# Kernel optimization log

Measured on AMD Instinct MI355X. Metric: run time of the kernel, lower is better.

Reference implementation:

```python
import jax, jax.numpy as jnp
import numpy as np
from jax import lax

N, CIN, P, CH, COUT = 1024, 3, 14, 256, 3
DN = ('NCHW', 'OIHW', 'NCHW')


def _conv(x, w, b, pad=1):
    y = lax.conv_general_dilated(x, w, (1, 1), [(pad, pad), (pad, pad)], dimension_numbers=DN)
    return y + b[None, :, None, None]


def _conv_transpose(x, w_t, b):
    # PyTorch ConvTranspose2d(k=3, stride=2, padding=1, output_padding=1):
    # equivalent to conv with lhs_dilation=2, padding (k-1-p, k-1-p+op) = (1, 2),
    # kernel with in/out swapped and spatially flipped. w_t: [in, out, 3, 3]
    w = jnp.flip(jnp.transpose(w_t, (1, 0, 2, 3)), axis=(2, 3))  # [out, in, 3, 3]
    y = lax.conv_general_dilated(x, w, (1, 1), [(1, 2), (1, 2)], lhs_dilation=(2, 2),
                                 dimension_numbers=DN)
    return y + b[None, :, None, None]


def setup_inputs() -> dict:
    key = jax.random.key(0)
    ks = jax.random.split(key, 16)
    s3 = lambda cin: 1.0 / np.sqrt(cin * 9)
    inp = {"x": jax.random.normal(ks[0], (N, CIN, P, P), dtype=jnp.float32)}
    inp["w1"] = jax.random.normal(ks[1], (CH, CIN, 3, 3), jnp.float32) * s3(CIN)
    inp["b1"] = jnp.zeros((CH,), jnp.float32)
    inp["w2"] = jax.random.normal(ks[2], (CH, CH, 3, 3), jnp.float32) * s3(CH)
    inp["b2"] = jnp.zeros((CH,), jnp.float32)
    inp["w3"] = jax.random.normal(ks[3], (CH, CH, 3, 3), jnp.float32) * s3(CH)
    inp["b3"] = jnp.zeros((CH,), jnp.float32)
    inp["w4"] = jax.random.normal(ks[4], (CH, CH, 3, 3), jnp.float32) * s3(CH)
    inp["b4"] = jnp.zeros((CH,), jnp.float32)
    inp["wt"] = jax.random.normal(ks[5], (CH, CH, 3, 3), jnp.float32) * s3(CH)  # [in, out, kh, kw]
    inp["bt"] = jnp.zeros((CH,), jnp.float32)
    inp["w5"] = jax.random.normal(ks[6], (COUT, CH, 1, 1), jnp.float32) * (1.0 / np.sqrt(CH))
    inp["b5"] = jnp.zeros((COUT,), jnp.float32)
    return inp


def reference(x, w1, b1, w2, b2, w3, b3, w4, b4, wt, bt, w5, b5):
    h = jax.nn.relu(_conv(x, w1, b1))
    h = jax.nn.relu(_conv(h, w2, b2))
    h = jax.nn.relu(_conv(h, w3, b3))
    h = jax.nn.relu(_conv(h, w4, b4))
    h = jax.nn.relu(_conv_transpose(h, wt, bt))  # [N, 256, 2P, 2P]
    h = _conv(h, w5, b5, pad=0)                   # 1x1 conv -> [N, 3, 2P, 2P]
    return jax.nn.sigmoid(h)
```

## Files before the change

### kernel.cpp

```cpp
#include <hip/hip_runtime.h>
#include <hip/hip_fp16.h>

typedef _Float16 half8 __attribute__((ext_vector_type(8)));
typedef _Float16 half4 __attribute__((ext_vector_type(4)));
typedef float floatx4 __attribute__((ext_vector_type(4)));

#define PLANE 65536
#define PK_ELEMS 589824
#define GUARD 4096

__global__ void repack_kernel(const float* __restrict__ w2, const float* __restrict__ w3,
                              const float* __restrict__ w4, const float* __restrict__ wt,
                              _Float16* __restrict__ pk) {
    int t = blockIdx.x * 256 + threadIdx.x;
    int l = t & 63;
    int idx = t >> 6;
    int nt = idx & 15; idx >>= 4;
    int ks = idx & 7;  idx >>= 3;
    int tap = idx % 9;
    int layer = idx / 9;
    int co = nt * 16 + (l & 15);
    int ci0 = ks * 32 + (l >> 4) * 8;
    const float* w = (layer == 0) ? w2 : (layer == 1) ? w3 : (layer == 2) ? w4 : wt;
    _Float16* dst = pk + (size_t)layer * PK_ELEMS + (((size_t)(tap * 8 + ks) * 16 + nt) * 64 + l) * 8;
    if (layer < 3) {
        for (int j = 0; j < 8; ++j)
            dst[j] = (_Float16)w[(co * 256 + (ci0 + j)) * 9 + tap];
    } else {
        int ky = tap / 3, kx = tap % 3;
        for (int j = 0; j < 8; ++j)
            dst[j] = (_Float16)w[((ci0 + j) * 256 + co) * 9 + (2 - ky) * 3 + (2 - kx)];
    }
}

__global__ __launch_bounds__(1024, 4) void conv1_kernel(const float* __restrict__ x,
                                                        const float* __restrict__ w1,
                                                        const float* __restrict__ b1,
                                                        _Float16* __restrict__ act) {
    __shared__ float inl[3][16][16];
    __shared__ float lw[256 * 27];
    __shared__ float lb1[256];
    int n = blockIdx.x, tid = threadIdx.x;
    if (tid < 768) ((float*)inl)[tid] = 0.f;
    __syncthreads();
    for (int i = tid; i < 3 * 196; i += 1024) {
        int ci = i / 196, r = i % 196, y = r / 14, xx = r % 14;
        inl[ci][y + 1][xx + 1] = x[(size_t)n * 588 + i];
    }
    for (int i = tid; i < 256 * 27; i += 1024) lw[i] = w1[i];
    if (tid < 256) lb1[tid] = b1[tid];
    __syncthreads();
    int p = tid >> 2, q = tid & 3;
    int py = p >> 4, px = p & 15;
    _Float16* ga = act + (size_t)n * PLANE + p * 256;
    int sw = (p & 7) << 3;
    if (py == 0 || py == 15 || px == 0 || px == 15) {
        for (int ci = 0; ci < 64; ++ci) { int co = q + ci * 4; ga[co ^ sw] = (_Float16)0.f; }
    } else {
        float vin[27];
        #pragma unroll
        for (int ci = 0; ci < 3; ++ci)
            #pragma unroll
            for (int ky = 0; ky < 3; ++ky)
                #pragma unroll
                for (int kx = 0; kx < 3; ++kx)
                    vin[ci * 9 + ky * 3 + kx] = inl[ci][py - 1 + ky][px - 1 + kx];
        for (int ci = 0; ci < 64; ++ci) {
            int co = q + ci * 4;
            float acc = lb1[co];
            const float* wp = &lw[co * 27];
            #pragma unroll
            for (int k = 0; k < 27; ++k) acc += vin[k] * wp[k];
            ga[co ^ sw] = (_Float16)fmaxf(acc, 0.f);
        }
    }
}


#define INIT_ACC(BIASPTR)                                                        \
    {                                                                            \
        _Pragma("unroll")                                                        \
        for (int ni = 0; ni < 4; ++ni) {                                         \
            floatx4 bv;                                                          \
            _Pragma("unroll")                                                    \
            for (int reg = 0; reg < 4; ++reg)                                    \
                bv[reg] = (BIASPTR)[(cg * 4 + ni) * 16 + kg * 4 + reg];          \
            _Pragma("unroll")                                                    \
            for (int i = 0; i < 5; ++i) acc[i][ni] = bv;                         \
        }                                                                        \
    }

#define ACCUM_TAP(PKT, DOFF)                                                     \
    {                                                                            \
        const _Float16* pkt_ = (PKT);                                            \
        int poff_[5];                                                            \
        _Pragma("unroll")                                                        \
        for (int j = 0; j < 5; ++j) poff_[j] = (pp[j] + (DOFF)) * 256;           \
        half8 a_[4], an_[4], bb_[5];                                             \
        _Pragma("unroll")                                                        \
        for (int ni = 0; ni < 4; ++ni)                                           \
            a_[ni] = *(const half8*)(pkt_ + ((cg * 4 + ni) * 64 + lane) * 8);    \
        _Pragma("clang loop unroll(disable)")                                    \
        for (int ks = 0; ks < 8; ++ks) {                                         \
            int kk = (ks * 4 + kg) << 3;                                         \
            _Pragma("unroll")                                                    \
            for (int j = 0; j < 4; ++j)                                          \
                bb_[j] = *(const half8*)(plane + poff_[j] + (kk ^ ((poff_[j] >> 5) & 56))); \
            if (pg == 0 || pg == 1)                                              \
                bb_[4] = *(const half8*)(plane + poff_[4] + (kk ^ ((poff_[4] >> 5) & 56))); \
            if (ks < 7) {                                                        \
                _Pragma("unroll")                                                \
                for (int ni = 0; ni < 4; ++ni)                                   \
                    an_[ni] = *(const half8*)(pkt_ + (((ks + 1) * 16 + cg * 4 + ni) * 64 + lane) * 8); \
            }                                                                    \
            _Pragma("unroll")                                                    \
            for (int j = 0; j < 4; ++j) {                                        \
                acc[j][0] = __builtin_amdgcn_mfma_f32_16x16x32_f16(a_[0], bb_[j], acc[j][0], 0, 0, 0); \
                acc[j][1] = __builtin_amdgcn_mfma_f32_16x16x32_f16(a_[1], bb_[j], acc[j][1], 0, 0, 0); \
                acc[j][2] = __builtin_amdgcn_mfma_f32_16x16x32_f16(a_[2], bb_[j], acc[j][2], 0, 0, 0); \
                acc[j][3] = __builtin_amdgcn_mfma_f32_16x16x32_f16(a_[3], bb_[j], acc[j][3], 0, 0, 0); \
            }                                                                    \
            if (pg == 0 || pg == 1) {                                            \
                acc[4][0] = __builtin_amdgcn_mfma_f32_16x16x32_f16(a_[0], bb_[4], acc[4][0], 0, 0, 0); \
                acc[4][1] = __builtin_amdgcn_mfma_f32_16x16x32_f16(a_[1], bb_[4], acc[4][1], 0, 0, 0); \
                acc[4][2] = __builtin_amdgcn_mfma_f32_16x16x32_f16(a_[2], bb_[4], acc[4][2], 0, 0, 0); \
                acc[4][3] = __builtin_amdgcn_mfma_f32_16x16x32_f16(a_[3], bb_[4], acc[4][3], 0, 0, 0); \
            }                                                                    \
            if (ks < 7) {                                                        \
                _Pragma("unroll")                                                \
                for (int ni = 0; ni < 4; ++ni) a_[ni] = an_[ni];                 \
            }                                                                    \
        }                                                                        \
    }

#define EPILOGUE(RY, RX)                                                         \
    {                                                                            \
        _Pragma("unroll")                                                        \
        for (int i = 0; i < 5; ++i) {                                            \
            if (i < 4 || pg < 2) {                                               \
                float s0 = 0.f, s1 = 0.f, s2 = 0.f;                              \
                _Pragma("unroll")                                                \
                for (int ni = 0; ni < 4; ++ni) {                                 \
                    int co0 = (cg * 4 + ni) * 16 + kg * 4;                       \
                    _Pragma("unroll")                                            \
                    for (int reg = 0; reg < 4; ++reg) {                          \
                        float v = fmaxf(acc[i][ni][reg], 0.f);                   \
                        s0 += v * w5l[co0 + reg];                                \
                        s1 += v * w5l[256 + co0 + reg];                          \
                        s2 += v * w5l[512 + co0 + reg];                          \
                    }                                                            \
                }                                                                \
                s0 += __shfl_xor(s0, 16, 64); s0 += __shfl_xor(s0, 32, 64);      \
                s1 += __shfl_xor(s1, 16, 64); s1 += __shfl_xor(s1, 32, 64);      \
                s2 += __shfl_xor(s2, 16, 64); s2 += __shfl_xor(s2, 32, 64);      \
                if (lane < 16 && colok) {                                        \
                    int yy = pg + 3 * i;                              \
                    int pix = (2 * yy + (RY)) * 28 + 2 * (col - 1) + (RX);       \
                    atomicAdd(&o3[pix * 3 + 0], s0);                             \
                    atomicAdd(&o3[pix * 3 + 1], s1);                             \
                    atomicAdd(&o3[pix * 3 + 2], s2);                             \
                }                                                                \
            }                                                                    \
        }                                                                        \
    }

__global__ __launch_bounds__(768, 3) void fused_kernel(const _Float16* __restrict__ act,
                                                       const _Float16* __restrict__ pk,
                                                       const float* __restrict__ b2,
                                                       const float* __restrict__ b3,
                                                       const float* __restrict__ b4,
                                                       const float* __restrict__ bt,
                                                       const float* __restrict__ w5,
                                                       const float* __restrict__ b5,
                                                       float* __restrict__ out) {
    __shared__ _Float16 plane[PLANE + 2 * GUARD];
    __shared__ float o3[2352];
    __shared__ float w5l[768];
    int n = blockIdx.x, tid = threadIdx.x;
    const _Float16* ga = act + (size_t)n * PLANE;
    if (tid < 512) {
        int g = (tid < 256) ? tid : (tid - 256 + (PLANE + GUARD) / 8);
        *(uint4*)(plane + g * 8) = uint4{0, 0, 0, 0};
    }
    for (int i = tid; i < 8192; i += 768)
        *(uint4*)(plane + GUARD + i * 8) = *(const uint4*)(ga + i * 8);
    for (int i = tid; i < 2352; i += 768) o3[i] = b5[i % 3];
    w5l[tid] = w5[tid];

    int lane = tid & 63, wid = tid >> 6;
    int cg = wid & 3, pg = wid >> 2;
    int col = lane & 15, kg = lane >> 4;
    bool colok = (col >= 1 && col <= 14);

    int pp[5];
    #pragma unroll
    for (int i = 0; i < 5; ++i) pp[i] = (pg + 3 * i + 1) * 16 + col + 16;
    __syncthreads();

    floatx4 acc[5][4];

    for (int L = 0; L < 3; ++L) {
        const _Float16* pkL = pk + (size_t)L * PK_ELEMS;
        const float* bias = (L == 0) ? b2 : (L == 1) ? b3 : b4;
        INIT_ACC(bias)
        for (int tap = 0; tap < 9; ++tap) {
            int doff = (tap / 3) * 16 + (tap % 3) - 17;
            ACCUM_TAP(pkL + (size_t)tap * 65536, doff)
        }
        __syncthreads();
        #pragma unroll
        for (int i = 0; i < 5; ++i) {
            if (i < 4 || pg < 2) {
                int ppix = pp[i];
                int sw = (ppix & 7) << 3;
                if (colok) {
                    #pragma unroll
                    for (int ni = 0; ni < 4; ++ni) {
                        int co0 = (cg * 4 + ni) * 16 + kg * 4;
                        half4 h;
                        #pragma unroll
                        for (int reg = 0; reg < 4; ++reg) h[reg] = (_Float16)fmaxf(acc[i][ni][reg], 0.f);
                        *(half4*)(plane + ppix * 256 + (co0 ^ sw)) = h;
                    }
                }
            }
        }
        __syncthreads();
    }

    const _Float16* pkT = pk + (size_t)3 * PK_ELEMS;
    INIT_ACC(bt)
    ACCUM_TAP(pkT + 4 * 65536, 0)
    EPILOGUE(0, 0)
    INIT_ACC(bt)
    ACCUM_TAP(pkT + 3 * 65536, 0)
    ACCUM_TAP(pkT + 5 * 65536, 1)
    EPILOGUE(0, 1)
    INIT_ACC(bt)
    ACCUM_TAP(pkT + 1 * 65536, 0)
    ACCUM_TAP(pkT + 7 * 65536, 16)
    EPILOGUE(1, 0)
    INIT_ACC(bt)
    ACCUM_TAP(pkT + 0 * 65536, 0)
    ACCUM_TAP(pkT + 2 * 65536, 1)
    ACCUM_TAP(pkT + 6 * 65536, 16)
    ACCUM_TAP(pkT + 8 * 65536, 17)
    EPILOGUE(1, 1)

    __syncthreads();
    size_t ob = (size_t)n * 2352;
    for (int i = tid; i < 2352; i += 768) {
        int pix = i / 3, c = i % 3;
        float v = o3[i];
        out[ob + (size_t)c * 784 + pix] = 1.f / (1.f + __expf(-v));
    }
}

extern "C" void kernel_launch(void* const* d_in, const int* in_sizes, int n_in,
                              void* d_out, int out_size, void* d_ws, size_t ws_size,
                              hipStream_t stream) {
    const float* x  = (const float*)d_in[0];
    const float* w1 = (const float*)d_in[1];
    const float* b1 = (const float*)d_in[2];
    const float* w2 = (const float*)d_in[3];
    const float* b2 = (const float*)d_in[4];
    const float* w3 = (const float*)d_in[5];
    const float* b3 = (const float*)d_in[6];
    const float* w4 = (const float*)d_in[7];
    const float* b4 = (const float*)d_in[8];
    const float* wt = (const float*)d_in[9];
    const float* bt = (const float*)d_in[10];
    const float* w5 = (const float*)d_in[11];
    const float* b5 = (const float*)d_in[12];

    size_t need = ((size_t)1024 * PLANE + 4 * (size_t)PK_ELEMS) * sizeof(_Float16);
    if (ws_size < need) return;

    _Float16* act = (_Float16*)d_ws;
    _Float16* pk  = act + (size_t)1024 * PLANE;

    repack_kernel<<<1152, 256, 0, stream>>>(w2, w3, w4, wt, pk);
    conv1_kernel<<<1024, 1024, 0, stream>>>(x, w1, b1, act);
    fused_kernel<<<1024, 768, 0, stream>>>(act, pk, b2, b3, b4, bt, w5, b5, (float*)d_out);
}
```

Before: 1.026 ms.

## Switch fused conv MFMA tiles from 16x16x32 to 32x32x16 with repacked weights

Replaces the 16x16x32 f16 MFMA tiling with 32x32x16 instructions. Each wave now covers 64 output channels as two 32-wide tiles and two image rows per 32-pixel tile. The weight repack layout, accumulator shapes, bias init, LDS writeback and epilogue reduction are all reworked to match the new register layout, and weight loads are prefetched two k-steps ahead. The aim is fewer instructions and less LDS operand traffic per FLOP, at the cost of larger accumulator register pressure and extra wasted work on row edges.

New measurement: 1.292 ms. +26.0%, slower.

```diff
diff --git a/kernel.cpp b/kernel.cpp
--- a/kernel.cpp
+++ b/kernel.cpp
@@ -3,7 +3,7 @@
 
 typedef _Float16 half8 __attribute__((ext_vector_type(8)));
 typedef _Float16 half4 __attribute__((ext_vector_type(4)));
-typedef float floatx4 __attribute__((ext_vector_type(4)));
+typedef float floatx16 __attribute__((ext_vector_type(16)));
 
 #define PLANE 65536
 #define PK_ELEMS 589824
@@ -15,14 +15,14 @@
     int t = blockIdx.x * 256 + threadIdx.x;
     int l = t & 63;
     int idx = t >> 6;
-    int nt = idx & 15; idx >>= 4;
-    int ks = idx & 7;  idx >>= 3;
+    int ct = idx & 7;  idx >>= 3;
+    int ks = idx & 15; idx >>= 4;
     int tap = idx % 9;
     int layer = idx / 9;
-    int co = nt * 16 + (l & 15);
-    int ci0 = ks * 32 + (l >> 4) * 8;
+    int co  = ct * 32 + (l & 31);
+    int ci0 = ks * 16 + (l >> 5) * 8;
     const float* w = (layer == 0) ? w2 : (layer == 1) ? w3 : (layer == 2) ? w4 : wt;
-    _Float16* dst = pk + (size_t)layer * PK_ELEMS + (((size_t)(tap * 8 + ks) * 16 + nt) * 64 + l) * 8;
+    _Float16* dst = pk + (size_t)layer * PK_ELEMS + (((size_t)(tap * 16 + ks) * 8 + ct) * 64 + l) * 8;
     if (layer < 3) {
         for (int j = 0; j < 8; ++j)
             dst[j] = (_Float16)w[(co * 256 + (ci0 + j)) * 9 + tap];
@@ -80,55 +80,55 @@
 #define INIT_ACC(BIASPTR)                                                        \
     {                                                                            \
         _Pragma("unroll")                                                        \
-        for (int ni = 0; ni < 4; ++ni) {                                         \
-            floatx4 bv;                                                          \
+        for (int c = 0; c < 2; ++c) {                                            \
+            floatx16 bv;                                                         \
             _Pragma("unroll")                                                    \
-            for (int reg = 0; reg < 4; ++reg)                                    \
-                bv[reg] = (BIASPTR)[(cg * 4 + ni) * 16 + kg * 4 + reg];          \
-            _Pragma("unroll")                                                    \
-            for (int i = 0; i < 5; ++i) acc[i][ni] = bv;                         \
+            for (int reg = 0; reg < 16; ++reg)                                   \
+                bv[reg] = (BIASPTR)[(cg * 2 + c) * 32 + 4 * h + (reg & 3) + 8 * (reg >> 2)]; \
+            acc[0][c] = bv; acc[1][c] = bv; acc[2][c] = bv;                      \
         }                                                                        \
     }
 
 #define ACCUM_TAP(PKT, DOFF)                                                     \
     {                                                                            \
         const _Float16* pkt_ = (PKT);                                            \
-        int poff_[5];                                                            \
-        _Pragma("unroll")                                                        \
-        for (int j = 0; j < 5; ++j) poff_[j] = (pp[j] + (DOFF)) * 256;           \
-        half8 a_[4], an_[4], bb_[5];                                             \
-        _Pragma("unroll")                                                        \
-        for (int ni = 0; ni < 4; ++ni)                                           \
-            a_[ni] = *(const half8*)(pkt_ + ((cg * 4 + ni) * 64 + lane) * 8);    \
+        int poff_[3], swj_[3];                                                   \
+        _Pragma("unroll")                                                        \
+        for (int j = 0; j < 3; ++j) {                                            \
+            poff_[j] = (pp[j] + (DOFF)) * 256;                                   \
+            swj_[j] = (poff_[j] >> 5) & 56;                                      \
+        }                                                                        \
+        half8 a_[2], an_[2], a2_[2], bb_[3];                                     \
+        _Pragma("unroll")                                                        \
+        for (int c = 0; c < 2; ++c) {                                            \
+            a_[c]  = *(const half8*)(pkt_ + ((cg * 2 + c) * 64 + lane) * 8);     \
+            an_[c] = *(const half8*)(pkt_ + (((8) + cg * 2 + c) * 64 + lane) * 8); \
+        }                                                                        \
         _Pragma("clang loop unroll(disable)")                                    \
-        for (int ks = 0; ks < 8; ++ks) {                                         \
-            int kk = (ks * 4 + kg) << 3;                                         \
-            _Pragma("unroll")                                                    \
-            for (int j = 0; j < 4; ++j)                                          \
-                bb_[j] = *(const half8*)(plane + poff_[j] + (kk ^ ((poff_[j] >> 5) & 56))); \
-            if (pg == 0 || pg == 1)                                              \
-                bb_[4] = *(const half8*)(plane + poff_[4] + (kk ^ ((poff_[4] >> 5) & 56))); \
-            if (ks < 7) {                                                        \
+        for (int ks = 0; ks < 16; ++ks) {                                        \
+            int kk = ks * 16 + h8;                                               \
+            bb_[0] = *(const half8*)(plane + poff_[0] + (kk ^ swj_[0]));         \
+            bb_[1] = *(const half8*)(plane + poff_[1] + (kk ^ swj_[1]));         \
+            if (pg == 0)                                                         \
+                bb_[2] = *(const half8*)(plane + poff_[2] + (kk ^ swj_[2]));     \
+            if (ks < 14) {                                                       \
                 _Pragma("unroll")                                                \
-                for (int ni = 0; ni < 4; ++ni)                                   \
-                    an_[ni] = *(const half8*)(pkt_ + (((ks + 1) * 16 + cg * 4 + ni) * 64 + lane) * 8); \
-            }                                                                    \
-            _Pragma("unroll")                                                    \
-            for (int j = 0; j < 4; ++j) {                                        \
-                acc[j][0] = __builtin_amdgcn_mfma_f32_16x16x32_f16(a_[0], bb_[j], acc[j][0], 0, 0, 0); \
-                acc[j][1] = __builtin_amdgcn_mfma_f32_16x16x32_f16(a_[1], bb_[j], acc[j][1], 0, 0, 0); \
-                acc[j][2] = __builtin_amdgcn_mfma_f32_16x16x32_f16(a_[2], bb_[j], acc[j][2], 0, 0, 0); \
-                acc[j][3] = __builtin_amdgcn_mfma_f32_16x16x32_f16(a_[3], bb_[j], acc[j][3], 0, 0, 0); \
-            }                                                                    \
-            if (pg == 0 || pg == 1) {                                            \
-                acc[4][0] = __builtin_amdgcn_mfma_f32_16x16x32_f16(a_[0], bb_[4], acc[4][0], 0, 0, 0); \
-                acc[4][1] = __builtin_amdgcn_mfma_f32_16x16x32_f16(a_[1], bb_[4], acc[4][1], 0, 0, 0); \
-                acc[4][2] = __builtin_amdgcn_mfma_f32_16x16x32_f16(a_[2], bb_[4], acc[4][2], 0, 0, 0); \
-                acc[4][3] = __builtin_amdgcn_mfma_f32_16x16x32_f16(a_[3], bb_[4], acc[4][3], 0, 0, 0); \
-            }                                                                    \
-            if (ks < 7) {                                                        \
-                _Pragma("unroll")                                                \
-                for (int ni = 0; ni < 4; ++ni) a_[ni] = an_[ni];                 \
+                for (int c = 0; c < 2; ++c)                                      \
+                    a2_[c] = *(const half8*)(pkt_ + (((ks + 2) * 8 + cg * 2 + c) * 64 + lane) * 8); \
+            }                                                                    \
+            acc[0][0] = __builtin_amdgcn_mfma_f32_32x32x16_f16(a_[0], bb_[0], acc[0][0], 0, 0, 0); \
+            acc[0][1] = __builtin_amdgcn_mfma_f32_32x32x16_f16(a_[1], bb_[0], acc[0][1], 0, 0, 0); \
+            acc[1][0] = __builtin_amdgcn_mfma_f32_32x32x16_f16(a_[0], bb_[1], acc[1][0], 0, 0, 0); \
+            acc[1][1] = __builtin_amdgcn_mfma_f32_32x32x16_f16(a_[1], bb_[1], acc[1][1], 0, 0, 0); \
+            if (pg == 0) {                                                       \
+                acc[2][0] = __builtin_amdgcn_mfma_f32_32x32x16_f16(a_[0], bb_[2], acc[2][0], 0, 0, 0); \
+                acc[2][1] = __builtin_amdgcn_mfma_f32_32x32x16_f16(a_[1], bb_[2], acc[2][1], 0, 0, 0); \
+            }                                                                    \
+            if (ks < 14) {                                                       \
+                a_[0] = an_[0]; a_[1] = an_[1];                                  \
+                an_[0] = a2_[0]; an_[1] = a2_[1];                                \
+            } else {                                                             \
+                a_[0] = an_[0]; a_[1] = an_[1];                                  \
             }                                                                    \
         }                                                                        \
     }
@@ -136,25 +136,26 @@
 #define EPILOGUE(RY, RX)                                                         \
     {                                                                            \
         _Pragma("unroll")                                                        \
-        for (int i = 0; i < 5; ++i) {                                            \
-            if (i < 4 || pg < 2) {                                               \
+        for (int i = 0; i < 3; ++i) {                                            \
+            if (i < 2 || pg == 0) {                                              \
                 float s0 = 0.f, s1 = 0.f, s2 = 0.f;                              \
                 _Pragma("unroll")                                                \
-                for (int ni = 0; ni < 4; ++ni) {                                 \
-                    int co0 = (cg * 4 + ni) * 16 + kg * 4;                       \
+                for (int c = 0; c < 2; ++c) {                                    \
+                    int cb = (cg * 2 + c) * 32 + 4 * h;                          \
                     _Pragma("unroll")                                            \
-                    for (int reg = 0; reg < 4; ++reg) {                          \
-                        float v = fmaxf(acc[i][ni][reg], 0.f);                   \
-                        s0 += v * w5l[co0 + reg];                                \
-                        s1 += v * w5l[256 + co0 + reg];                          \
-                        s2 += v * w5l[512 + co0 + reg];                          \
+                    for (int reg = 0; reg < 16; ++reg) {                         \
+                        int co = cb + (reg & 3) + 8 * (reg >> 2);                \
+                        float v = fmaxf(acc[i][c][reg], 0.f);                    \
+                        s0 += v * w5l[co];                                       \
+                        s1 += v * w5l[256 + co];                                 \
+                        s2 += v * w5l[512 + co];                                 \
                     }                                                            \
                 }                                                                \
-                s0 += __shfl_xor(s0, 16, 64); s0 += __shfl_xor(s0, 32, 64);      \
-                s1 += __shfl_xor(s1, 16, 64); s1 += __shfl_xor(s1, 32, 64);      \
-                s2 += __shfl_xor(s2, 16, 64); s2 += __shfl_xor(s2, 32, 64);      \
-                if (lane < 16 && colok) {                                        \
-                    int yy = pg + 3 * i;                              \
+                s0 += __shfl_xor(s0, 32, 64);                                    \
+                s1 += __shfl_xor(s1, 32, 64);                                    \
+                s2 += __shfl_xor(s2, 32, 64);                                    \
+                if (lane < 32 && colok) {                                        \
+                    int yy = 2 * (pg + 3 * i) + ((lane >> 4) & 1);               \
                     int pix = (2 * yy + (RY)) * 28 + 2 * (col - 1) + (RX);       \
                     atomicAdd(&o3[pix * 3 + 0], s0);                             \
                     atomicAdd(&o3[pix * 3 + 1], s1);                             \
@@ -178,9 +179,9 @@
     __shared__ float w5l[768];
     int n = blockIdx.x, tid = threadIdx.x;
     const _Float16* ga = act + (size_t)n * PLANE;
-    if (tid < 512) {
-        int g = (tid < 256) ? tid : (tid - 256 + (PLANE + GUARD) / 8);
-        *(uint4*)(plane + g * 8) = uint4{0, 0, 0, 0};
+    for (int i = tid; i < 1024; i += 768) {
+        int e = (i < 512) ? i : (i - 512) + (GUARD + PLANE) / 8;
+        *(uint4*)(plane + e * 8) = uint4{0, 0, 0, 0};
     }
     for (int i = tid; i < 8192; i += 768)
         *(uint4*)(plane + GUARD + i * 8) = *(const uint4*)(ga + i * 8);
@@ -189,15 +190,19 @@
 
     int lane = tid & 63, wid = tid >> 6;
     int cg = wid & 3, pg = wid >> 2;
-    int col = lane & 15, kg = lane >> 4;
+    int col = lane & 15;
+    int h = lane >> 5, h8 = h * 8;
     bool colok = (col >= 1 && col <= 14);
 
-    int pp[5];
+    int pp[3];
     #pragma unroll
-    for (int i = 0; i < 5; ++i) pp[i] = (pg + 3 * i + 1) * 16 + col + 16;
-    __syncthreads();
-
-    floatx4 acc[5][4];
+    for (int i = 0; i < 3; ++i) {
+        int t = pg + 3 * i;
+        pp[i] = (2 * t + 1 + ((lane >> 4) & 1)) * 16 + col + 16;
+    }
+    __syncthreads();
+
+    floatx16 acc[3][2];
 
     for (int L = 0; L < 3; ++L) {
         const _Float16* pkL = pk + (size_t)L * PK_ELEMS;
@@ -209,18 +214,22 @@
         }
         __syncthreads();
         #pragma unroll
-        for (int i = 0; i < 5; ++i) {
-            if (i < 4 || pg < 2) {
+        for (int i = 0; i < 3; ++i) {
+            if (i < 2 || pg == 0) {
                 int ppix = pp[i];
                 int sw = (ppix & 7) << 3;
                 if (colok) {
                     #pragma unroll
-                    for (int ni = 0; ni < 4; ++ni) {
-                        int co0 = (cg * 4 + ni) * 16 + kg * 4;
-                        half4 h;
+                    for (int c = 0; c < 2; ++c) {
+                        int cb = (cg * 2 + c) * 32 + 4 * h;
                         #pragma unroll
-                        for (int reg = 0; reg < 4; ++reg) h[reg] = (_Float16)fmaxf(acc[i][ni][reg], 0.f);
-                        *(half4*)(plane + ppix * 256 + (co0 ^ sw)) = h;
+                        for (int g = 0; g < 4; ++g) {
+                            int co0 = cb + 8 * g;
+                            half4 hv;
+                            #pragma unroll
+                            for (int r = 0; r < 4; ++r) hv[r] = (_Float16)fmaxf(acc[i][c][4 * g + r], 0.f);
+                            *(half4*)(plane + ppix * 256 + (co0 ^ sw)) = hv;
+                        }
                     }
                 }
             }
```
